# Performance work log

Measured on AMD Instinct MI355X. Metric: run time of the kernel, lower is better.

## Reference

```python
import jax, jax.numpy as jnp
import numpy as np

IN_FEATURES = 4096
OUT_FEATURES = 11008
GROUP_SIZE = 128
N_HIGH = 1024   # int(0.25*4096)//8*8
N_LOW = 3072    # (4096-1024)//8*8
M_TOKENS = 64


def unpack_6bit(packed, original_k):
    # packed: [K*3//4, N] uint8 values stored as int32
    _, N = packed.shape
    p = packed.reshape(original_k // 4, 3, N)
    b0, b1, b2 = p[:, 0], p[:, 1], p[:, 2]
    v0 = b0 & 63
    v1 = ((b0 >> 6) & 3) | ((b1 & 15) << 2)
    v2 = ((b1 >> 4) & 15) | ((b2 & 3) << 4)
    v3 = (b2 >> 2) & 63
    return jnp.stack([v0, v1, v2, v3], axis=1).reshape(original_k, N)


def unpack_5bit(packed, original_k):
    # packed: [K*5//8, N]
    _, N = packed.shape
    p = packed.reshape(original_k // 8, 5, N)
    b = [p[:, i] for i in range(5)]
    v0 = b[0] & 31
    v1 = ((b[0] >> 5) & 7) | ((b[1] & 3) << 3)
    v2 = (b[1] >> 2) & 31
    v3 = ((b[1] >> 7) & 1) | ((b[2] & 15) << 1)
    v4 = ((b[2] >> 4) & 15) | ((b[3] & 1) << 4)
    v5 = (b[3] >> 1) & 31
    v6 = ((b[3] >> 6) & 3) | ((b[4] & 7) << 2)
    v7 = (b[4] >> 3) & 31
    return jnp.stack([v0, v1, v2, v3, v4, v5, v6, v7], axis=1).reshape(original_k, N)


def dequant_region(W_q, scales, half_range):
    # W_q: [K, N] ints in [0, 2*half_range]; scales: [num_groups, N]
    K, N = W_q.shape
    G = scales.shape[0]
    Wg = (W_q.astype(jnp.float32) - float(half_range)).reshape(G, GROUP_SIZE, N)
    return (Wg * scales[:, None, :]).reshape(K, N)


def setup_inputs() -> dict:
    key = jax.random.key(0)
    ks = jax.random.split(key, 7)
    x = jax.random.normal(ks[0], (M_TOKENS, IN_FEATURES), dtype=jnp.float32)
    W_high_packed = jax.random.randint(ks[1], (N_HIGH * 3 // 4, OUT_FEATURES), 0, 256, dtype=jnp.int32)
    W_low_packed = jax.random.randint(ks[2], (N_LOW * 5 // 8, OUT_FEATURES), 0, 256, dtype=jnp.int32)
    scales_high = jax.random.uniform(ks[3], (N_HIGH // GROUP_SIZE, OUT_FEATURES), dtype=jnp.float32) * 0.02 + 1e-4
    scales_low = jax.random.uniform(ks[4], (N_LOW // GROUP_SIZE, OUT_FEATURES), dtype=jnp.float32) * 0.02 + 1e-4
    col_indices = jax.random.permutation(ks[5], IN_FEATURES).astype(jnp.int32)
    bias = jax.random.normal(ks[6], (OUT_FEATURES,), dtype=jnp.float32) * 0.02
    return {"x": x, "W_high_packed": W_high_packed, "W_low_packed": W_low_packed,
            "scales_high": scales_high, "scales_low": scales_low,
            "col_indices": col_indices, "bias": bias}


def reference(x, W_high_packed, W_low_packed, scales_high, scales_low, col_indices, bias):
    # Unpack mixed 6-bit / 5-bit weights and group-dequantize.
    Wq_high = unpack_6bit(W_high_packed, N_HIGH)          # [1024, N], 0..63
    Wq_low = unpack_5bit(W_low_packed, N_LOW)             # [3072, N], 0..31
    W_high = dequant_region(Wq_high, scales_high, 31)     # 6-bit half_range = 31
    W_low = dequant_region(Wq_low, scales_low, 15)        # 5-bit half_range = 15
    # Column-sensitivity reorder of activations, then split high/low regions.
    x_perm = x[:, col_indices]                            # [M, K]
    x_high = x_perm[:, :N_HIGH]
    x_low = x_perm[:, N_HIGH:N_HIGH + N_LOW]
    out = x_high @ W_high + x_low @ W_low + bias          # [M, N]
    return out
```

## Files before the change

kernel.cpp:

```cpp
#include <hip/hip_runtime.h>


#define NFEAT 11008
#define KTOT  4096

typedef _Float16 half8 __attribute__((ext_vector_type(8)));
typedef float    f32x4 __attribute__((ext_vector_type(4)));

__global__ __launch_bounds__(256) void prep_xfrag(const float* __restrict__ x,
                                                  const int* __restrict__ col,
                                                  _Float16* __restrict__ xfrag) {
    int idx = blockIdx.x * 256 + threadIdx.x;
    int j  = idx & 7;
    int l  = (idx >> 3) & 63;
    int mt = (idx >> 9) & 3;
    int s  = idx >> 11;
    int k  = s * 32 + ((l >> 4) << 3) + j;
    int m  = mt * 16 + (l & 15);
    xfrag[idx] = (_Float16)x[m * KTOT + col[k]];
}

__global__ __launch_bounds__(256) void gemm_kernel(const int* __restrict__ Wh,
                                                   const int* __restrict__ Wl,
                                                   const float* __restrict__ sh,
                                                   const float* __restrict__ sl,
                                                   const _Float16* __restrict__ xfrag,
                                                   float* __restrict__ dst,
                                                   int atomic_mode) {
    const int n0   = blockIdx.x * 64;
    const int kc   = blockIdx.y;
    const int tid  = threadIdx.x;
    const int lane = tid & 63;
    const int wave = tid >> 6;

    __shared__ _Float16 Wfrag[8 * 64 * 8 + 4 * 8];

    f32x4 acc[4];
#pragma unroll
    for (int i = 0; i < 4; ++i) acc[i] = (f32x4){0.f, 0.f, 0.f, 0.f};

    const int col  = lane;
    const int nt   = col >> 4;
    const int n_in = col & 15;

    for (int t = 0; t < 16; ++t) {
        if (kc == 0) {
            const float s = sh[(t >> 1) * NFEAT + n0 + col];
#pragma unroll
            for (int p = 0; p < 2; ++p) {
                const int kg2 = p * 4 + wave;
                const int k   = t * 64 + kg2 * 8;
                const int G   = k >> 2;
                const int* bp = Wh + (3 * G) * NFEAT + n0 + col;
                int b0 = bp[0],         b1 = bp[NFEAT],     b2 = bp[2 * NFEAT];
                int b3 = bp[3 * NFEAT], b4 = bp[4 * NFEAT], b5 = bp[5 * NFEAT];
                int v[8];
                v[0] = b0 & 63;
                v[1] = ((b0 >> 6) & 3) | ((b1 & 15) << 2);
                v[2] = ((b1 >> 4) & 15) | ((b2 & 3) << 4);
                v[3] = (b2 >> 2) & 63;
                v[4] = b3 & 63;
                v[5] = ((b3 >> 6) & 3) | ((b4 & 15) << 2);
                v[6] = ((b4 >> 4) & 15) | ((b5 & 3) << 4);
                v[7] = (b5 >> 2) & 63;
                half8 w;
#pragma unroll
                for (int j = 0; j < 8; ++j) w[j] = (_Float16)(((float)v[j] - 31.0f) * s);
                const int q = kg2 >> 2, quad = kg2 & 3;
                const int off = (((nt * 2 + q) * 64 + quad * 16 + n_in) + nt) * 8;
                *(half8*)&Wfrag[off] = w;
            }
        } else {
            const int kl0 = (kc - 1) * 1024 + t * 64;
            const float s = sl[(kl0 >> 7) * NFEAT + n0 + col];
#pragma unroll
            for (int p = 0; p < 2; ++p) {
                const int kg8 = p * 4 + wave;
                const int kl  = kl0 + kg8 * 8;
                const int G   = kl >> 3;
                const int* bp = Wl + (5 * G) * NFEAT + n0 + col;
                int b0 = bp[0], b1 = bp[NFEAT], b2 = bp[2 * NFEAT];
                int b3 = bp[3 * NFEAT], b4 = bp[4 * NFEAT];
                int v[8];
                v[0] = b0 & 31;
                v[1] = ((b0 >> 5) & 7) | ((b1 & 3) << 3);
                v[2] = (b1 >> 2) & 31;
                v[3] = ((b1 >> 7) & 1) | ((b2 & 15) << 1);
                v[4] = ((b2 >> 4) & 15) | ((b3 & 1) << 4);
                v[5] = (b3 >> 1) & 31;
                v[6] = ((b3 >> 6) & 3) | ((b4 & 7) << 2);
                v[7] = (b4 >> 3) & 31;
                half8 w;
#pragma unroll
                for (int j = 0; j < 8; ++j) w[j] = (_Float16)(((float)v[j] - 15.0f) * s);
                const int q = kg8 >> 2, quad = kg8 & 3;
                const int off = (((nt * 2 + q) * 64 + quad * 16 + n_in) + nt) * 8;
                *(half8*)&Wfrag[off] = w;
            }
        }
        __syncthreads();

#pragma unroll
        for (int q = 0; q < 2; ++q) {
            const int sg = kc * 32 + t * 2 + q;
            half8 a = *(const half8*)(xfrag + (((sg * 4 + wave) * 64 + lane) << 3));
#pragma unroll
            for (int j = 0; j < 4; ++j) {
                half8 b = *(half8*)&Wfrag[(((j * 2 + q) * 64 + lane) + j) * 8];
                acc[j] = __builtin_amdgcn_mfma_f32_16x16x32_f16(a, b, acc[j], 0, 0, 0);
            }
        }
        __syncthreads();
    }

    const int rb = wave * 16 + ((lane >> 4) << 2);
    const int cb = lane & 15;
    if (atomic_mode) {
#pragma unroll
        for (int j = 0; j < 4; ++j)
#pragma unroll
            for (int r = 0; r < 4; ++r)
                atomicAdd(&dst[(rb + r) * NFEAT + n0 + j * 16 + cb], acc[j][r]);
    } else {
        float* base = dst + (size_t)kc * 64 * NFEAT;
#pragma unroll
        for (int j = 0; j < 4; ++j)
#pragma unroll
            for (int r = 0; r < 4; ++r)
                base[(rb + r) * NFEAT + n0 + j * 16 + cb] = acc[j][r];
    }
}

__global__ __launch_bounds__(256) void reduce_out(const float* __restrict__ part,
                                                  const float* __restrict__ bias,
                                                  float* __restrict__ out) {
    const int idx = blockIdx.x * 256 + threadIdx.x;
    const int f   = idx * 4;
    const int n   = f % NFEAT;
    f32x4 a = *(const f32x4*)(part + f);
    f32x4 b = *(const f32x4*)(part + 704512 + f);
    f32x4 c = *(const f32x4*)(part + 2 * 704512 + f);
    f32x4 d = *(const f32x4*)(part + 3 * 704512 + f);
    f32x4 bi = *(const f32x4*)(bias + n);
    *(f32x4*)(out + f) = a + b + c + d + bi;
}

__global__ __launch_bounds__(256) void init_bias(const float* __restrict__ bias,
                                                 float* __restrict__ out) {
    const int idx = blockIdx.x * 256 + threadIdx.x;
    out[idx] = bias[idx % NFEAT];
}

extern "C" void kernel_launch(void* const* d_in, const int* in_sizes, int n_in,
                              void* d_out, int out_size, void* d_ws, size_t ws_size,
                              hipStream_t stream) {
    const float* x    = (const float*)d_in[0];
    const int*   Wh   = (const int*)d_in[1];
    const int*   Wl   = (const int*)d_in[2];
    const float* sh   = (const float*)d_in[3];
    const float* sl   = (const float*)d_in[4];
    const int*   col  = (const int*)d_in[5];
    const float* bias = (const float*)d_in[6];
    float* out = (float*)d_out;

    _Float16* xfrag = (_Float16*)d_ws;
    const size_t xfrag_bytes = 64 * KTOT * sizeof(_Float16);
    const size_t part_bytes  = 4ull * 64 * NFEAT * sizeof(float);

    prep_xfrag<<<1024, 256, 0, stream>>>(x, col, xfrag);

    dim3 grid(172, 4);
    if (ws_size >= xfrag_bytes + part_bytes) {
        float* part = (float*)((char*)d_ws + xfrag_bytes);
        gemm_kernel<<<grid, 256, 0, stream>>>(Wh, Wl, sh, sl, xfrag, part, 0);
        reduce_out<<<688, 256, 0, stream>>>(part, bias, out);
    } else {
        init_bias<<<2752, 256, 0, stream>>>(bias, out);
        gemm_kernel<<<grid, 256, 0, stream>>>(Wh, Wl, sh, sl, xfrag, out, 1);
    }
}
```

Baseline: 176.7 us.

## Double-buffer dequantized weights, prefetch packed words, split K across eight waves

The GEMM block grows to 512 threads. Each of the eight waves now dequantizes one 8-row k-group per step and computes MFMAs for half of the K-substeps. Packed weight words and scales for the next step are loaded into registers while the current step is processed. The LDS weight tile is double-buffered, so only one barrier per iteration is needed instead of two. At the end the two wave halves combine partial accumulators through LDS before the store, which adds an extra reduction pass and more register and LDS pressure per block.

Result: no change. 175.0 us (-1.0%).

```diff
diff --git a/kernel.cpp b/kernel.cpp
--- a/kernel.cpp
+++ b/kernel.cpp
@@ -20,7 +20,7 @@
     xfrag[idx] = (_Float16)x[m * KTOT + col[k]];
 }
 
-__global__ __launch_bounds__(256) void gemm_kernel(const int* __restrict__ Wh,
+__global__ __launch_bounds__(512) void gemm_kernel(const int* __restrict__ Wh,
                                                    const int* __restrict__ Wl,
                                                    const float* __restrict__ sh,
                                                    const float* __restrict__ sl,
@@ -33,7 +33,7 @@
     const int lane = tid & 63;
     const int wave = tid >> 6;
 
-    __shared__ _Float16 Wfrag[8 * 64 * 8 + 4 * 8];
+    __shared__ _Float16 Wfrag[2][8 * 64 * 8 + 4 * 8];
 
     f32x4 acc[4];
 #pragma unroll
@@ -42,92 +42,134 @@
     const int col  = lane;
     const int nt   = col >> 4;
     const int n_in = col & 15;
-
-    for (int t = 0; t < 16; ++t) {
-        if (kc == 0) {
-            const float s = sh[(t >> 1) * NFEAT + n0 + col];
-#pragma unroll
-            for (int p = 0; p < 2; ++p) {
-                const int kg2 = p * 4 + wave;
-                const int k   = t * 64 + kg2 * 8;
-                const int G   = k >> 2;
-                const int* bp = Wh + (3 * G) * NFEAT + n0 + col;
-                int b0 = bp[0],         b1 = bp[NFEAT],     b2 = bp[2 * NFEAT];
-                int b3 = bp[3 * NFEAT], b4 = bp[4 * NFEAT], b5 = bp[5 * NFEAT];
-                int v[8];
-                v[0] = b0 & 63;
-                v[1] = ((b0 >> 6) & 3) | ((b1 & 15) << 2);
-                v[2] = ((b1 >> 4) & 15) | ((b2 & 3) << 4);
-                v[3] = (b2 >> 2) & 63;
-                v[4] = b3 & 63;
-                v[5] = ((b3 >> 6) & 3) | ((b4 & 15) << 2);
-                v[6] = ((b4 >> 4) & 15) | ((b5 & 3) << 4);
-                v[7] = (b5 >> 2) & 63;
-                half8 w;
-#pragma unroll
-                for (int j = 0; j < 8; ++j) w[j] = (_Float16)(((float)v[j] - 31.0f) * s);
-                const int q = kg2 >> 2, quad = kg2 & 3;
-                const int off = (((nt * 2 + q) * 64 + quad * 16 + n_in) + nt) * 8;
-                *(half8*)&Wfrag[off] = w;
+    const int kg   = wave;
+    const int q_w  = kg >> 2, quad = kg & 3;
+    const int woff = (((nt * 2 + q_w) * 64 + quad * 16 + n_in) + nt) * 8;
+
+    const int mt = wave & 3;
+    const int qm = wave >> 2;
+
+    auto mfma_step = [&](int t) {
+        const int sg = kc * 32 + t * 2 + qm;
+        half8 a = *(const half8*)(xfrag + (((sg * 4 + mt) * 64 + lane) << 3));
+        const _Float16* wf = Wfrag[t & 1];
+#pragma unroll
+        for (int j = 0; j < 4; ++j) {
+            half8 b = *(const half8*)&wf[(((j * 2 + qm) * 64 + lane) + j) * 8];
+            acc[j] = __builtin_amdgcn_mfma_f32_16x16x32_f16(a, b, acc[j], 0, 0, 0);
+        }
+    };
+
+    if (kc == 0) {
+        const int*   base  = Wh + n0 + col;
+        const float* sbase = sh + n0 + col;
+        int c0, c1, c2, c3, c4, c5; float cs;
+        {
+            const int* bp = base + 3 * (kg * 2) * NFEAT;
+            c0 = bp[0];         c1 = bp[NFEAT];     c2 = bp[2 * NFEAT];
+            c3 = bp[3 * NFEAT]; c4 = bp[4 * NFEAT]; c5 = bp[5 * NFEAT];
+            cs = sbase[0];
+        }
+#pragma unroll 2
+        for (int t = 0; t < 16; ++t) {
+            int n_0 = 0, n_1 = 0, n_2 = 0, n_3 = 0, n_4 = 0, n_5 = 0; float ns = 0.f;
+            if (t + 1 < 16) {
+                const int G = (t + 1) * 16 + kg * 2;
+                const int* bp = base + 3 * G * NFEAT;
+                n_0 = bp[0];         n_1 = bp[NFEAT];     n_2 = bp[2 * NFEAT];
+                n_3 = bp[3 * NFEAT]; n_4 = bp[4 * NFEAT]; n_5 = bp[5 * NFEAT];
+                ns = sbase[((t + 1) >> 1) * NFEAT];
             }
+            int v[8];
+            v[0] = c0 & 63;
+            v[1] = ((c0 >> 6) & 3) | ((c1 & 15) << 2);
+            v[2] = ((c1 >> 4) & 15) | ((c2 & 3) << 4);
+            v[3] = (c2 >> 2) & 63;
+            v[4] = c3 & 63;
+            v[5] = ((c3 >> 6) & 3) | ((c4 & 15) << 2);
+            v[6] = ((c4 >> 4) & 15) | ((c5 & 3) << 4);
+            v[7] = (c5 >> 2) & 63;
+            half8 w;
+#pragma unroll
+            for (int j = 0; j < 8; ++j) w[j] = (_Float16)(((float)v[j] - 31.0f) * cs);
+            *(half8*)&Wfrag[t & 1][woff] = w;
+            __syncthreads();
+            mfma_step(t);
+            c0 = n_0; c1 = n_1; c2 = n_2; c3 = n_3; c4 = n_4; c5 = n_5; cs = ns;
+        }
+    } else {
+        const int*   base  = Wl + n0 + col;
+        const float* sbase = sl + n0 + col;
+        const int Gbase = (kc - 1) * 128;
+        const int sbase_row = (kc - 1) * 8;
+        int c0, c1, c2, c3, c4; float cs;
+        {
+            const int* bp = base + 5 * (Gbase + kg) * NFEAT;
+            c0 = bp[0]; c1 = bp[NFEAT]; c2 = bp[2 * NFEAT];
+            c3 = bp[3 * NFEAT]; c4 = bp[4 * NFEAT];
+            cs = sbase[sbase_row * NFEAT];
+        }
+#pragma unroll 2
+        for (int t = 0; t < 16; ++t) {
+            int n_0 = 0, n_1 = 0, n_2 = 0, n_3 = 0, n_4 = 0; float ns = 0.f;
+            if (t + 1 < 16) {
+                const int* bp = base + 5 * (Gbase + (t + 1) * 8 + kg) * NFEAT;
+                n_0 = bp[0]; n_1 = bp[NFEAT]; n_2 = bp[2 * NFEAT];
+                n_3 = bp[3 * NFEAT]; n_4 = bp[4 * NFEAT];
+                ns = sbase[(sbase_row + ((t + 1) >> 1)) * NFEAT];
+            }
+            int v[8];
+            v[0] = c0 & 31;
+            v[1] = ((c0 >> 5) & 7) | ((c1 & 3) << 3);
+            v[2] = (c1 >> 2) & 31;
+            v[3] = ((c1 >> 7) & 1) | ((c2 & 15) << 1);
+            v[4] = ((c2 >> 4) & 15) | ((c3 & 1) << 4);
+            v[5] = (c3 >> 1) & 31;
+            v[6] = ((c3 >> 6) & 3) | ((c4 & 7) << 2);
+            v[7] = (c4 >> 3) & 31;
+            half8 w;
+#pragma unroll
+            for (int j = 0; j < 8; ++j) w[j] = (_Float16)(((float)v[j] - 15.0f) * cs);
+            *(half8*)&Wfrag[t & 1][woff] = w;
+            __syncthreads();
+            mfma_step(t);
+            c0 = n_0; c1 = n_1; c2 = n_2; c3 = n_3; c4 = n_4; cs = ns;
+        }
+    }
+
+    __syncthreads();
+    float* red = (float*)&Wfrag[0][0];
+    if (wave >= 4) {
+#pragma unroll
+        for (int j = 0; j < 4; ++j)
+#pragma unroll
+            for (int r = 0; r < 4; ++r)
+                red[(j * 4 + r) * 256 + (wave - 4) * 64 + lane] = acc[j][r];
+    }
+    __syncthreads();
+    if (wave < 4) {
+#pragma unroll
+        for (int j = 0; j < 4; ++j)
+#pragma unroll
+            for (int r = 0; r < 4; ++r)
+                acc[j][r] += red[(j * 4 + r) * 256 + wave * 64 + lane];
+
+        const int rb = wave * 16 + ((lane >> 4) << 2);
+        const int cb = lane & 15;
+        if (atomic_mode) {
+#pragma unroll
+            for (int j = 0; j < 4; ++j)
+#pragma unroll
+                for (int r = 0; r < 4; ++r)
+                    atomicAdd(&dst[(rb + r) * NFEAT + n0 + j * 16 + cb], acc[j][r]);
         } else {
-            const int kl0 = (kc - 1) * 1024 + t * 64;
-            const float s = sl[(kl0 >> 7) * NFEAT + n0 + col];
-#pragma unroll
-            for (int p = 0; p < 2; ++p) {
-                const int kg8 = p * 4 + wave;
-                const int kl  = kl0 + kg8 * 8;
-                const int G   = kl >> 3;
-                const int* bp = Wl + (5 * G) * NFEAT + n0 + col;
-                int b0 = bp[0], b1 = bp[NFEAT], b2 = bp[2 * NFEAT];
-                int b3 = bp[3 * NFEAT], b4 = bp[4 * NFEAT];
-                int v[8];
-                v[0] = b0 & 31;
-                v[1] = ((b0 >> 5) & 7) | ((b1 & 3) << 3);
-                v[2] = (b1 >> 2) & 31;
-                v[3] = ((b1 >> 7) & 1) | ((b2 & 15) << 1);
-                v[4] = ((b2 >> 4) & 15) | ((b3 & 1) << 4);
-                v[5] = (b3 >> 1) & 31;
-                v[6] = ((b3 >> 6) & 3) | ((b4 & 7) << 2);
-                v[7] = (b4 >> 3) & 31;
-                half8 w;
-#pragma unroll
-                for (int j = 0; j < 8; ++j) w[j] = (_Float16)(((float)v[j] - 15.0f) * s);
-                const int q = kg8 >> 2, quad = kg8 & 3;
-                const int off = (((nt * 2 + q) * 64 + quad * 16 + n_in) + nt) * 8;
-                *(half8*)&Wfrag[off] = w;
-            }
-        }
-        __syncthreads();
-
-#pragma unroll
-        for (int q = 0; q < 2; ++q) {
-            const int sg = kc * 32 + t * 2 + q;
-            half8 a = *(const half8*)(xfrag + (((sg * 4 + wave) * 64 + lane) << 3));
-#pragma unroll
-            for (int j = 0; j < 4; ++j) {
-                half8 b = *(half8*)&Wfrag[(((j * 2 + q) * 64 + lane) + j) * 8];
-                acc[j] = __builtin_amdgcn_mfma_f32_16x16x32_f16(a, b, acc[j], 0, 0, 0);
-            }
-        }
-        __syncthreads();
-    }
-
-    const int rb = wave * 16 + ((lane >> 4) << 2);
-    const int cb = lane & 15;
-    if (atomic_mode) {
-#pragma unroll
-        for (int j = 0; j < 4; ++j)
-#pragma unroll
-            for (int r = 0; r < 4; ++r)
-                atomicAdd(&dst[(rb + r) * NFEAT + n0 + j * 16 + cb], acc[j][r]);
-    } else {
-        float* base = dst + (size_t)kc * 64 * NFEAT;
-#pragma unroll
-        for (int j = 0; j < 4; ++j)
-#pragma unroll
-            for (int r = 0; r < 4; ++r)
-                base[(rb + r) * NFEAT + n0 + j * 16 + cb] = acc[j][r];
+            float* base = dst + (size_t)kc * 64 * NFEAT;
+#pragma unroll
+            for (int j = 0; j < 4; ++j)
+#pragma unroll
+                for (int r = 0; r < 4; ++r)
+                    base[(rb + r) * NFEAT + n0 + j * 16 + cb] = acc[j][r];
+        }
     }
 }
 
@@ -172,10 +214,10 @@
     dim3 grid(172, 4);
     if (ws_size >= xfrag_bytes + part_bytes) {
         float* part = (float*)((char*)d_ws + xfrag_bytes);
-        gemm_kernel<<<grid, 256, 0, stream>>>(Wh, Wl, sh, sl, xfrag, part, 0);
+        gemm_kernel<<<grid, 512, 0, stream>>>(Wh, Wl, sh, sl, xfrag, part, 0);
         reduce_out<<<688, 256, 0, stream>>>(part, bias, out);
     } else {
         init_bias<<<2752, 256, 0, stream>>>(bias, out);
-        gemm_kernel<<<grid, 256, 0, stream>>>(Wh, Wl, sh, sl, xfrag, out, 1);
-    }
-}
+        gemm_kernel<<<grid, 512, 0, stream>>>(Wh, Wl, sh, sl, xfrag, out, 1);
+    }
+}
```

## Dequantize weights directly into MFMA B registers and split K eight ways

Applied to the files above, without the earlier changes.

Each wave now owns its own 16 output columns and dequantizes packed weights straight into the MFMA B operand registers. This removes the shared-memory staging buffer and both __syncthreads per step. The K dimension is split into 8 chunks instead of 4, which doubles the grid to 1376 blocks for better CU occupancy, and reduce_out takes a variable partial count. Dequantization uses a single fma with a precomputed offset. The trade-off is that every wave reloads all four x fragments from global memory per step, and the partial buffer written and reduced is twice as large.

New measurement: 193.3 us. 1.09x slower.

```diff
diff --git a/kernel.cpp b/kernel.cpp
--- a/kernel.cpp
+++ b/kernel.cpp
@@ -20,129 +20,133 @@
     xfrag[idx] = (_Float16)x[m * KTOT + col[k]];
 }
 
-__global__ __launch_bounds__(256) void gemm_kernel(const int* __restrict__ Wh,
-                                                   const int* __restrict__ Wl,
-                                                   const float* __restrict__ sh,
-                                                   const float* __restrict__ sl,
-                                                   const _Float16* __restrict__ xfrag,
-                                                   float* __restrict__ dst,
-                                                   int atomic_mode) {
+__global__ __launch_bounds__(256, 4) void gemm_kernel(const int* __restrict__ Wh,
+                                                      const int* __restrict__ Wl,
+                                                      const float* __restrict__ sh,
+                                                      const float* __restrict__ sl,
+                                                      const _Float16* __restrict__ xfrag,
+                                                      float* __restrict__ dst,
+                                                      int atomic_mode) {
     const int n0   = blockIdx.x * 64;
     const int kc   = blockIdx.y;
-    const int tid  = threadIdx.x;
-    const int lane = tid & 63;
-    const int wave = tid >> 6;
+    const int klen = KTOT / gridDim.y;
+    const int k0   = kc * klen;
+    const int lane = threadIdx.x & 63;
+    const int wave = threadIdx.x >> 6;
 
-    __shared__ _Float16 Wfrag[8 * 64 * 8 + 4 * 8];
+    const int n  = n0 + wave * 16 + (lane & 15);
+    const int kb = (lane >> 4) << 3;
 
     f32x4 acc[4];
 #pragma unroll
     for (int i = 0; i < 4; ++i) acc[i] = (f32x4){0.f, 0.f, 0.f, 0.f};
 
-    const int col  = lane;
-    const int nt   = col >> 4;
-    const int n_in = col & 15;
+    const int ngroups = klen >> 7;
 
-    for (int t = 0; t < 16; ++t) {
-        if (kc == 0) {
-            const float s = sh[(t >> 1) * NFEAT + n0 + col];
+    if (k0 < 1024) {
+        for (int g = 0; g < ngroups; ++g) {
+            const float s    = sh[((k0 >> 7) + g) * NFEAT + n];
+            const float moff = -31.0f * s;
 #pragma unroll
-            for (int p = 0; p < 2; ++p) {
-                const int kg2 = p * 4 + wave;
-                const int k   = t * 64 + kg2 * 8;
-                const int G   = k >> 2;
-                const int* bp = Wh + (3 * G) * NFEAT + n0 + col;
-                int b0 = bp[0],         b1 = bp[NFEAT],     b2 = bp[2 * NFEAT];
-                int b3 = bp[3 * NFEAT], b4 = bp[4 * NFEAT], b5 = bp[5 * NFEAT];
-                int v[8];
-                v[0] = b0 & 63;
-                v[1] = ((b0 >> 6) & 3) | ((b1 & 15) << 2);
-                v[2] = ((b1 >> 4) & 15) | ((b2 & 3) << 4);
-                v[3] = (b2 >> 2) & 63;
-                v[4] = b3 & 63;
-                v[5] = ((b3 >> 6) & 3) | ((b4 & 15) << 2);
-                v[6] = ((b4 >> 4) & 15) | ((b5 & 3) << 4);
-                v[7] = (b5 >> 2) & 63;
-                half8 w;
+            for (int st = 0; st < 4; ++st) {
+                const int k = k0 + g * 128 + st * 32 + kb;
+                const int G = k >> 2;
+                const int* bp = Wh + 3 * G * NFEAT + n;
+                const int b0 = bp[0];         const int b1 = bp[NFEAT];
+                const int b2 = bp[2 * NFEAT]; const int b3 = bp[3 * NFEAT];
+                const int b4 = bp[4 * NFEAT]; const int b5 = bp[5 * NFEAT];
+                int v0 = b0 & 63;
+                int v1 = ((b0 >> 6) & 3) | ((b1 & 15) << 2);
+                int v2 = ((b1 >> 4) & 15) | ((b2 & 3) << 4);
+                int v3 = (b2 >> 2) & 63;
+                int v4 = b3 & 63;
+                int v5 = ((b3 >> 6) & 3) | ((b4 & 15) << 2);
+                int v6 = ((b4 >> 4) & 15) | ((b5 & 3) << 4);
+                int v7 = (b5 >> 2) & 63;
+                half8 b;
+                b[0] = (_Float16)fmaf((float)v0, s, moff);
+                b[1] = (_Float16)fmaf((float)v1, s, moff);
+                b[2] = (_Float16)fmaf((float)v2, s, moff);
+                b[3] = (_Float16)fmaf((float)v3, s, moff);
+                b[4] = (_Float16)fmaf((float)v4, s, moff);
+                b[5] = (_Float16)fmaf((float)v5, s, moff);
+                b[6] = (_Float16)fmaf((float)v6, s, moff);
+                b[7] = (_Float16)fmaf((float)v7, s, moff);
+                const int sg = (k0 >> 5) + g * 4 + st;
 #pragma unroll
-                for (int j = 0; j < 8; ++j) w[j] = (_Float16)(((float)v[j] - 31.0f) * s);
-                const int q = kg2 >> 2, quad = kg2 & 3;
-                const int off = (((nt * 2 + q) * 64 + quad * 16 + n_in) + nt) * 8;
-                *(half8*)&Wfrag[off] = w;
-            }
-        } else {
-            const int kl0 = (kc - 1) * 1024 + t * 64;
-            const float s = sl[(kl0 >> 7) * NFEAT + n0 + col];
-#pragma unroll
-            for (int p = 0; p < 2; ++p) {
-                const int kg8 = p * 4 + wave;
-                const int kl  = kl0 + kg8 * 8;
-                const int G   = kl >> 3;
-                const int* bp = Wl + (5 * G) * NFEAT + n0 + col;
-                int b0 = bp[0], b1 = bp[NFEAT], b2 = bp[2 * NFEAT];
-                int b3 = bp[3 * NFEAT], b4 = bp[4 * NFEAT];
-                int v[8];
-                v[0] = b0 & 31;
-                v[1] = ((b0 >> 5) & 7) | ((b1 & 3) << 3);
-                v[2] = (b1 >> 2) & 31;
-                v[3] = ((b1 >> 7) & 1) | ((b2 & 15) << 1);
-                v[4] = ((b2 >> 4) & 15) | ((b3 & 1) << 4);
-                v[5] = (b3 >> 1) & 31;
-                v[6] = ((b3 >> 6) & 3) | ((b4 & 7) << 2);
-                v[7] = (b4 >> 3) & 31;
-                half8 w;
-#pragma unroll
-                for (int j = 0; j < 8; ++j) w[j] = (_Float16)(((float)v[j] - 15.0f) * s);
-                const int q = kg8 >> 2, quad = kg8 & 3;
-                const int off = (((nt * 2 + q) * 64 + quad * 16 + n_in) + nt) * 8;
-                *(half8*)&Wfrag[off] = w;
+                for (int mt = 0; mt < 4; ++mt) {
+                    half8 a = *(const half8*)(xfrag + (((sg * 4 + mt) * 64 + lane) << 3));
+                    acc[mt] = __builtin_amdgcn_mfma_f32_16x16x32_f16(a, b, acc[mt], 0, 0, 0);
+                }
             }
         }
-        __syncthreads();
-
+    } else {
+        const int kl0 = k0 - 1024;
+        for (int g = 0; g < ngroups; ++g) {
+            const float s    = sl[((kl0 >> 7) + g) * NFEAT + n];
+            const float moff = -15.0f * s;
 #pragma unroll
-        for (int q = 0; q < 2; ++q) {
-            const int sg = kc * 32 + t * 2 + q;
-            half8 a = *(const half8*)(xfrag + (((sg * 4 + wave) * 64 + lane) << 3));
+            for (int st = 0; st < 4; ++st) {
+                const int kl = kl0 + g * 128 + st * 32 + kb;
+                const int G8 = kl >> 3;
+                const int* bp = Wl + 5 * G8 * NFEAT + n;
+                const int b0 = bp[0];         const int b1 = bp[NFEAT];
+                const int b2 = bp[2 * NFEAT]; const int b3 = bp[3 * NFEAT];
+                const int b4 = bp[4 * NFEAT];
+                int v0 = b0 & 31;
+                int v1 = ((b0 >> 5) & 7) | ((b1 & 3) << 3);
+                int v2 = (b1 >> 2) & 31;
+                int v3 = ((b1 >> 7) & 1) | ((b2 & 15) << 1);
+                int v4 = ((b2 >> 4) & 15) | ((b3 & 1) << 4);
+                int v5 = (b3 >> 1) & 31;
+                int v6 = ((b3 >> 6) & 3) | ((b4 & 7) << 2);
+                int v7 = (b4 >> 3) & 31;
+                half8 b;
+                b[0] = (_Float16)fmaf((float)v0, s, moff);
+                b[1] = (_Float16)fmaf((float)v1, s, moff);
+                b[2] = (_Float16)fmaf((float)v2, s, moff);
+                b[3] = (_Float16)fmaf((float)v3, s, moff);
+                b[4] = (_Float16)fmaf((float)v4, s, moff);
+                b[5] = (_Float16)fmaf((float)v5, s, moff);
+                b[6] = (_Float16)fmaf((float)v6, s, moff);
+                b[7] = (_Float16)fmaf((float)v7, s, moff);
+                const int sg = 32 + (kl0 >> 5) + g * 4 + st;
 #pragma unroll
-            for (int j = 0; j < 4; ++j) {
-                half8 b = *(half8*)&Wfrag[(((j * 2 + q) * 64 + lane) + j) * 8];
-                acc[j] = __builtin_amdgcn_mfma_f32_16x16x32_f16(a, b, acc[j], 0, 0, 0);
+                for (int mt = 0; mt < 4; ++mt) {
+                    half8 a = *(const half8*)(xfrag + (((sg * 4 + mt) * 64 + lane) << 3));
+                    acc[mt] = __builtin_amdgcn_mfma_f32_16x16x32_f16(a, b, acc[mt], 0, 0, 0);
+                }
             }
         }
-        __syncthreads();
     }
 
-    const int rb = wave * 16 + ((lane >> 4) << 2);
-    const int cb = lane & 15;
+    const int r0 = (lane >> 4) << 2;
     if (atomic_mode) {
 #pragma unroll
-        for (int j = 0; j < 4; ++j)
+        for (int mt = 0; mt < 4; ++mt)
 #pragma unroll
             for (int r = 0; r < 4; ++r)
-                atomicAdd(&dst[(rb + r) * NFEAT + n0 + j * 16 + cb], acc[j][r]);
+                atomicAdd(&dst[(mt * 16 + r0 + r) * NFEAT + n], acc[mt][r]);
     } else {
         float* base = dst + (size_t)kc * 64 * NFEAT;
 #pragma unroll
-        for (int j = 0; j < 4; ++j)
+        for (int mt = 0; mt < 4; ++mt)
 #pragma unroll
             for (int r = 0; r < 4; ++r)
-                base[(rb + r) * NFEAT + n0 + j * 16 + cb] = acc[j][r];
+                base[(mt * 16 + r0 + r) * NFEAT + n] = acc[mt][r];
     }
 }
 
 __global__ __launch_bounds__(256) void reduce_out(const float* __restrict__ part,
                                                   const float* __restrict__ bias,
-                                                  float* __restrict__ out) {
+                                                  float* __restrict__ out, int nc) {
     const int idx = blockIdx.x * 256 + threadIdx.x;
     const int f   = idx * 4;
     const int n   = f % NFEAT;
-    f32x4 a = *(const f32x4*)(part + f);
-    f32x4 b = *(const f32x4*)(part + 704512 + f);
-    f32x4 c = *(const f32x4*)(part + 2 * 704512 + f);
-    f32x4 d = *(const f32x4*)(part + 3 * 704512 + f);
-    f32x4 bi = *(const f32x4*)(bias + n);
-    *(f32x4*)(out + f) = a + b + c + d + bi;
+    f32x4 sum = *(const f32x4*)(bias + n);
+    for (int c = 0; c < nc; ++c)
+        sum += *(const f32x4*)(part + (size_t)c * 704512 + f);
+    *(f32x4*)(out + f) = sum;
 }
 
 __global__ __launch_bounds__(256) void init_bias(const float* __restrict__ bias,
@@ -165,17 +169,20 @@
 
     _Float16* xfrag = (_Float16*)d_ws;
     const size_t xfrag_bytes = 64 * KTOT * sizeof(_Float16);
-    const size_t part_bytes  = 4ull * 64 * NFEAT * sizeof(float);
+    const size_t part1 = 64ull * NFEAT * sizeof(float);
 
     prep_xfrag<<<1024, 256, 0, stream>>>(x, col, xfrag);
 
-    dim3 grid(172, 4);
-    if (ws_size >= xfrag_bytes + part_bytes) {
+    if (ws_size >= xfrag_bytes + 8 * part1) {
         float* part = (float*)((char*)d_ws + xfrag_bytes);
-        gemm_kernel<<<grid, 256, 0, stream>>>(Wh, Wl, sh, sl, xfrag, part, 0);
-        reduce_out<<<688, 256, 0, stream>>>(part, bias, out);
+        gemm_kernel<<<dim3(172, 8), 256, 0, stream>>>(Wh, Wl, sh, sl, xfrag, part, 0);
+        reduce_out<<<688, 256, 0, stream>>>(part, bias, out, 8);
+    } else if (ws_size >= xfrag_bytes + 4 * part1) {
+        float* part = (float*)((char*)d_ws + xfrag_bytes);
+        gemm_kernel<<<dim3(172, 4), 256, 0, stream>>>(Wh, Wl, sh, sl, xfrag, part, 0);
+        reduce_out<<<688, 256, 0, stream>>>(part, bias, out, 4);
     } else {
         init_bias<<<2752, 256, 0, stream>>>(bias, out);
-        gemm_kernel<<<grid, 256, 0, stream>>>(Wh, Wl, sh, sl, xfrag, out, 1);
+        gemm_kernel<<<dim3(172, 8), 256, 0, stream>>>(Wh, Wl, sh, sl, xfrag, out, 1);
     }
 }
```
